# Kernel tuning notes

Hardware: AMD Instinct MI355X
Metric: run time of the kernel (lower is better)

The kernel has to match this reference:

```python
import jax, jax.numpy as jnp
import numpy as np

EPS = 1e-10

def setup_inputs() -> dict:
    key = jax.random.key(0)
    k1, k2, k3 = jax.random.split(key, 3)
    B, K, M, X, Y = 64, 4, 3, 256, 256
    predictions = jax.random.uniform(k1, (B, K, X, Y), dtype=jnp.float32)
    inputs = jax.random.normal(k2, (B, M, X, Y), dtype=jnp.float32)
    heart = jax.random.randint(k3, (B, 1, X, Y), 0, 2, dtype=jnp.int32)
    return {"predictions": predictions, "inputs": inputs, "heart": heart}

def reference(predictions, inputs, heart):
    B, K, X, Y = predictions.shape
    M = inputs.shape[1]
    P = X * Y
    pred = predictions.reshape(B, K, P)            # [B,K,P]
    inp = inputs.reshape(B, M, P)                  # [B,M,P]
    w = (heart.reshape(B, P) == 1).astype(pred.dtype)  # ROI mask [B,P]
    pw = pred * w[:, None, :]                      # masked responsibilities [B,K,P]
    s = pw.sum(-1) + EPS                           # [B,K]
    # weighted means/vars over masked pixels
    mu = jnp.einsum('bkp,bmp->bkm', pw, inp) / s[..., None]        # [B,K,M]
    diff = inp[:, None, :, :] - mu[..., None]                      # [B,K,M,P]
    var = jnp.einsum('bkmp,bkp->bkm', diff * diff, pw) / s[..., None] + EPS
    # per-channel Gaussian pdf, product over channels M
    pdf = jnp.exp(-diff * diff / (2.0 * var[..., None])) / jnp.sqrt(2.0 * jnp.pi * var)[..., None]
    temp = jnp.prod(pdf, axis=2)                   # [B,K,P]
    mix = jnp.sum(pred * temp, axis=1)             # [B,P]
    ll = jnp.log(mix + EPS)
    n = w.sum(-1)                                   # pixels in ROI per sample
    loss_b = -(ll * w).sum(-1) / n                 # mean over masked pixels
    return jnp.mean(loss_b)
```

## Files before the change

kernel.cpp:

```cpp
#include <hip/hip_runtime.h>

#define EPS 1e-10f

constexpr int B_ = 64, K_ = 4, M_ = 3, P_ = 65536;
constexpr int THREADS = 256;
constexpr int CHUNK = 2048;
constexpr int BPB = P_ / CHUNK;
constexpr int VPT = CHUNK / 4 / THREADS;
constexpr int NS = 32;
constexpr int NACC = 29;

__global__ __launch_bounds__(THREADS) void k_stats(
    const float* __restrict__ pred, const float* __restrict__ inp,
    const int* __restrict__ heart, float* __restrict__ sums)
{
    const int blk   = blockIdx.x;
    const int b     = blk / BPB;
    const int chunk = blk % BPB;
    const int tid   = threadIdx.x;

    const float4* pb = (const float4*)(pred + (size_t)b * K_ * P_);
    const float4* ib = (const float4*)(inp  + (size_t)b * M_ * P_);
    const int4*   hb = (const int4*)(heart + (size_t)b * P_);
    const int vbase = chunk * (CHUNK / 4);

    float sacc[K_], tacc[K_][M_], uacc[K_][M_], nacc = 0.f;
    #pragma unroll
    for (int k = 0; k < K_; ++k) {
        sacc[k] = 0.f;
        #pragma unroll
        for (int m = 0; m < M_; ++m) { tacc[k][m] = 0.f; uacc[k][m] = 0.f; }
    }

    #pragma unroll
    for (int it = 0; it < VPT; ++it) {
        const int v = vbase + it * THREADS + tid;
        const int4 h4 = hb[v];
        float4 pk[K_];
        float4 xm[M_];
        #pragma unroll
        for (int k = 0; k < K_; ++k) pk[k] = pb[k * (P_ / 4) + v];
        #pragma unroll
        for (int m = 0; m < M_; ++m) xm[m] = ib[m * (P_ / 4) + v];

        #define PIX1(C) do {                                                  \
            const float w = (h4.C == 1) ? 1.f : 0.f;                          \
            nacc += w;                                                        \
            _Pragma("unroll")                                                 \
            for (int k = 0; k < K_; ++k) {                                    \
                const float pw = pk[k].C * w;                                 \
                sacc[k] += pw;                                                \
                _Pragma("unroll")                                             \
                for (int m = 0; m < M_; ++m) {                                \
                    const float x = xm[m].C;                                  \
                    tacc[k][m] = fmaf(pw,     x, tacc[k][m]);                 \
                    uacc[k][m] = fmaf(pw * x, x, uacc[k][m]);                 \
                }                                                             \
            }                                                                 \
        } while (0)
        PIX1(x); PIX1(y); PIX1(z); PIX1(w);
        #undef PIX1
    }

    float acc[NACC];
    #pragma unroll
    for (int k = 0; k < K_; ++k) {
        acc[k] = sacc[k];
        #pragma unroll
        for (int m = 0; m < M_; ++m) {
            acc[4  + k * M_ + m] = tacc[k][m];
            acc[16 + k * M_ + m] = uacc[k][m];
        }
    }
    acc[28] = nacc;

    __shared__ float lds[4][NACC];
    const int lane = tid & 63, wid = tid >> 6;
    #pragma unroll
    for (int i = 0; i < NACC; ++i) {
        float x = acc[i];
        #pragma unroll
        for (int off = 32; off; off >>= 1) x += __shfl_down(x, off);
        if (lane == 0) lds[wid][i] = x;
    }
    __syncthreads();
    if (tid < NACC) {
        const float x = lds[0][tid] + lds[1][tid] + lds[2][tid] + lds[3][tid];
        atomicAdd(&sums[b * NS + tid], x);
    }
}

__global__ __launch_bounds__(THREADS) void k_loss(
    const float* __restrict__ pred, const float* __restrict__ inp,
    const int* __restrict__ heart, const float* __restrict__ sums,
    float* __restrict__ out)
{
    const int blk   = blockIdx.x;
    const int b     = blk / BPB;
    const int chunk = blk % BPB;
    const int tid   = threadIdx.x;

    const float* sb = sums + b * NS;
    float mu[K_][M_], iv[K_][M_], ck[K_];
    #pragma unroll
    for (int k = 0; k < K_; ++k) {
        const float s = sb[k] + EPS;
        const float inv_s = 1.f / s;
        float c = 1.f;
        #pragma unroll
        for (int m = 0; m < M_; ++m) {
            const float t = sb[4  + k * M_ + m];
            const float u = sb[16 + k * M_ + m];
            const float muv = t * inv_s;
            const float var = fmaf(-muv, muv, u * inv_s) + EPS;
            mu[k][m] = muv;
            iv[k][m] = 0.5f / var;
            c *= rsqrtf(6.283185307179586f * var);
        }
        ck[k] = c;
    }
    const float invn = 1.f / (sb[28] * (float)B_);

    const float4* pb = (const float4*)(pred + (size_t)b * K_ * P_);
    const float4* ib = (const float4*)(inp  + (size_t)b * M_ * P_);
    const int4*   hb = (const int4*)(heart + (size_t)b * P_);
    const int vbase = chunk * (CHUNK / 4);

    float part = 0.f;
    #pragma unroll
    for (int it = 0; it < VPT; ++it) {
        const int v = vbase + it * THREADS + tid;
        const int4 h4 = hb[v];
        float4 pk[K_];
        float4 xm[M_];
        #pragma unroll
        for (int k = 0; k < K_; ++k) pk[k] = pb[k * (P_ / 4) + v];
        #pragma unroll
        for (int m = 0; m < M_; ++m) xm[m] = ib[m * (P_ / 4) + v];

        #define PIX3(C) do {                                                  \
            const float w = (h4.C == 1) ? 1.f : 0.f;                          \
            float mix = EPS;                                                  \
            _Pragma("unroll")                                                 \
            for (int k = 0; k < K_; ++k) {                                    \
                float e = 0.f;                                                \
                _Pragma("unroll")                                             \
                for (int m = 0; m < M_; ++m) {                                \
                    const float d = xm[m].C - mu[k][m];                       \
                    e = fmaf(-(d * d), iv[k][m], e);                          \
                }                                                             \
                mix = fmaf(pk[k].C * ck[k], __expf(e), mix);                  \
            }                                                                 \
            part = fmaf(w, __logf(mix), part);                                \
        } while (0)
        PIX3(x); PIX3(y); PIX3(z); PIX3(w);
        #undef PIX3
    }

    __shared__ float lds[4];
    const int lane = tid & 63, wid = tid >> 6;
    float x = part;
    #pragma unroll
    for (int off = 32; off; off >>= 1) x += __shfl_down(x, off);
    if (lane == 0) lds[wid] = x;
    __syncthreads();
    if (tid == 0)
        atomicAdd(out, -(lds[0] + lds[1] + lds[2] + lds[3]) * invn);
}

extern "C" void kernel_launch(void* const* d_in, const int* in_sizes, int n_in,
                              void* d_out, int out_size, void* d_ws, size_t ws_size,
                              hipStream_t stream)
{
    const float* pred  = (const float*)d_in[0];
    const float* inp   = (const float*)d_in[1];
    const int*   heart = (const int*)d_in[2];
    float* out  = (float*)d_out;
    float* sums = (float*)d_ws;

    hipMemsetAsync(sums, 0, B_ * NS * sizeof(float), stream);
    hipMemsetAsync(out,  0, sizeof(float), stream);

    k_stats<<<B_ * BPB, THREADS, 0, stream>>>(pred, inp, heart, sums);
    k_loss <<<B_ * BPB, THREADS, 0, stream>>>(pred, inp, heart, sums, out);
}
```

Before: 76.10 us.

## Stage inputs through LDS with block-rotated plane order and smaller chunks

Both kernels now copy each 1024-pixel chunk of all eight planes (4 pred, 3 inp, heart) into shared memory. Each block starts at a different plane, chosen by a rotation from its block index, so concurrent blocks hit different DRAM channels and pages. Scheduling barriers keep the loads in issue order. The chunk is halved, so there are twice as many blocks and twice as many atomics. The extra LDS round-trip and 32KB of shared memory per block may reduce occupancy.

New measurement: 124.3 us. +63.4%, slower.

```diff
diff --git a/kernel.cpp b/kernel.cpp
--- a/kernel.cpp
+++ b/kernel.cpp
@@ -4,25 +4,48 @@
 
 constexpr int B_ = 64, K_ = 4, M_ = 3, P_ = 65536;
 constexpr int THREADS = 256;
-constexpr int CHUNK = 2048;
-constexpr int BPB = P_ / CHUNK;
-constexpr int VPT = CHUNK / 4 / THREADS;
+constexpr int CH = 1024;
+constexpr int NCH = P_ / CH;
 constexpr int NS = 32;
 constexpr int NACC = 29;
+
+__device__ __forceinline__ void stage_phases(
+    const float* __restrict__ pred, const float* __restrict__ inp,
+    const int* __restrict__ heart, int b, int px0, int rot,
+    float (*sbuf)[CH], int tid)
+{
+    #pragma unroll
+    for (int ph = 0; ph < 8; ++ph) {
+        const int pl = (ph + rot) & 7;
+        const float* g;
+        if (pl < 4)      g = pred + ((size_t)b * K_ + pl) * P_ + px0;
+        else if (pl < 7) g = inp  + ((size_t)b * M_ + (pl - 4)) * P_ + px0;
+        else             g = (const float*)(heart + (size_t)b * P_ + px0);
+        const float4 v = ((const float4*)g)[tid];
+        ((float4*)&sbuf[pl][0])[tid] = v;
+        __builtin_amdgcn_sched_barrier(0);
+    }
+}
 
 __global__ __launch_bounds__(THREADS) void k_stats(
     const float* __restrict__ pred, const float* __restrict__ inp,
     const int* __restrict__ heart, float* __restrict__ sums)
 {
-    const int blk   = blockIdx.x;
-    const int b     = blk / BPB;
-    const int chunk = blk % BPB;
+    __shared__ float sbuf[8][CH];
+    __shared__ float red[4][NACC];
+    const int b     = blockIdx.x / NCH;
+    const int chunk = blockIdx.x % NCH;
     const int tid   = threadIdx.x;
 
-    const float4* pb = (const float4*)(pred + (size_t)b * K_ * P_);
-    const float4* ib = (const float4*)(inp  + (size_t)b * M_ * P_);
-    const int4*   hb = (const int4*)(heart + (size_t)b * P_);
-    const int vbase = chunk * (CHUNK / 4);
+    stage_phases(pred, inp, heart, b, chunk * CH, blockIdx.x, sbuf, tid);
+    __syncthreads();
+
+    const int4 h4 = ((const int4*)&sbuf[7][0])[tid];
+    float4 pk[K_]; float4 xm[M_];
+    #pragma unroll
+    for (int k = 0; k < K_; ++k) pk[k] = ((const float4*)&sbuf[k][0])[tid];
+    #pragma unroll
+    for (int m = 0; m < M_; ++m) xm[m] = ((const float4*)&sbuf[4 + m][0])[tid];
 
     float sacc[K_], tacc[K_][M_], uacc[K_][M_], nacc = 0.f;
     #pragma unroll
@@ -32,35 +55,23 @@
         for (int m = 0; m < M_; ++m) { tacc[k][m] = 0.f; uacc[k][m] = 0.f; }
     }
 
-    #pragma unroll
-    for (int it = 0; it < VPT; ++it) {
-        const int v = vbase + it * THREADS + tid;
-        const int4 h4 = hb[v];
-        float4 pk[K_];
-        float4 xm[M_];
-        #pragma unroll
-        for (int k = 0; k < K_; ++k) pk[k] = pb[k * (P_ / 4) + v];
-        #pragma unroll
-        for (int m = 0; m < M_; ++m) xm[m] = ib[m * (P_ / 4) + v];
-
-        #define PIX1(C) do {                                                  \
-            const float w = (h4.C == 1) ? 1.f : 0.f;                          \
-            nacc += w;                                                        \
+    #define PIX1(C) do {                                                      \
+        const float w = (h4.C == 1) ? 1.f : 0.f;                              \
+        nacc += w;                                                            \
+        _Pragma("unroll")                                                     \
+        for (int k = 0; k < K_; ++k) {                                        \
+            const float pw = pk[k].C * w;                                     \
+            sacc[k] += pw;                                                    \
             _Pragma("unroll")                                                 \
-            for (int k = 0; k < K_; ++k) {                                    \
-                const float pw = pk[k].C * w;                                 \
-                sacc[k] += pw;                                                \
-                _Pragma("unroll")                                             \
-                for (int m = 0; m < M_; ++m) {                                \
-                    const float x = xm[m].C;                                  \
-                    tacc[k][m] = fmaf(pw,     x, tacc[k][m]);                 \
-                    uacc[k][m] = fmaf(pw * x, x, uacc[k][m]);                 \
-                }                                                             \
+            for (int m = 0; m < M_; ++m) {                                    \
+                const float x = xm[m].C;                                      \
+                tacc[k][m] = fmaf(pw,     x, tacc[k][m]);                     \
+                uacc[k][m] = fmaf(pw * x, x, uacc[k][m]);                     \
             }                                                                 \
-        } while (0)
-        PIX1(x); PIX1(y); PIX1(z); PIX1(w);
-        #undef PIX1
-    }
+        }                                                                     \
+    } while (0)
+    PIX1(x); PIX1(y); PIX1(z); PIX1(w);
+    #undef PIX1
 
     float acc[NACC];
     #pragma unroll
@@ -74,18 +85,17 @@
     }
     acc[28] = nacc;
 
-    __shared__ float lds[4][NACC];
     const int lane = tid & 63, wid = tid >> 6;
     #pragma unroll
     for (int i = 0; i < NACC; ++i) {
         float x = acc[i];
         #pragma unroll
         for (int off = 32; off; off >>= 1) x += __shfl_down(x, off);
-        if (lane == 0) lds[wid][i] = x;
+        if (lane == 0) red[wid][i] = x;
     }
     __syncthreads();
     if (tid < NACC) {
-        const float x = lds[0][tid] + lds[1][tid] + lds[2][tid] + lds[3][tid];
+        const float x = red[0][tid] + red[1][tid] + red[2][tid] + red[3][tid];
         atomicAdd(&sums[b * NS + tid], x);
     }
 }
@@ -95,9 +105,10 @@
     const int* __restrict__ heart, const float* __restrict__ sums,
     float* __restrict__ out)
 {
-    const int blk   = blockIdx.x;
-    const int b     = blk / BPB;
-    const int chunk = blk % BPB;
+    __shared__ float sbuf[8][CH];
+    __shared__ float red[4];
+    const int b     = blockIdx.x / NCH;
+    const int chunk = blockIdx.x % NCH;
     const int tid   = threadIdx.x;
 
     const float* sb = sums + b * NS;
@@ -121,51 +132,43 @@
     }
     const float invn = 1.f / (sb[28] * (float)B_);
 
-    const float4* pb = (const float4*)(pred + (size_t)b * K_ * P_);
-    const float4* ib = (const float4*)(inp  + (size_t)b * M_ * P_);
-    const int4*   hb = (const int4*)(heart + (size_t)b * P_);
-    const int vbase = chunk * (CHUNK / 4);
+    stage_phases(pred, inp, heart, b, chunk * CH, blockIdx.x, sbuf, tid);
+    __syncthreads();
+
+    const int4 h4 = ((const int4*)&sbuf[7][0])[tid];
+    float4 pk[K_]; float4 xm[M_];
+    #pragma unroll
+    for (int k = 0; k < K_; ++k) pk[k] = ((const float4*)&sbuf[k][0])[tid];
+    #pragma unroll
+    for (int m = 0; m < M_; ++m) xm[m] = ((const float4*)&sbuf[4 + m][0])[tid];
 
     float part = 0.f;
-    #pragma unroll
-    for (int it = 0; it < VPT; ++it) {
-        const int v = vbase + it * THREADS + tid;
-        const int4 h4 = hb[v];
-        float4 pk[K_];
-        float4 xm[M_];
-        #pragma unroll
-        for (int k = 0; k < K_; ++k) pk[k] = pb[k * (P_ / 4) + v];
-        #pragma unroll
-        for (int m = 0; m < M_; ++m) xm[m] = ib[m * (P_ / 4) + v];
+    #define PIX3(C) do {                                                      \
+        const float w = (h4.C == 1) ? 1.f : 0.f;                              \
+        float mix = EPS;                                                      \
+        _Pragma("unroll")                                                     \
+        for (int k = 0; k < K_; ++k) {                                        \
+            float e = 0.f;                                                    \
+            _Pragma("unroll")                                                 \
+            for (int m = 0; m < M_; ++m) {                                    \
+                const float d = xm[m].C - mu[k][m];                           \
+                e = fmaf(-(d * d), iv[k][m], e);                              \
+            }                                                                 \
+            mix = fmaf(pk[k].C * ck[k], __expf(e), mix);                      \
+        }                                                                     \
+        part = fmaf(w, __logf(mix), part);                                    \
+    } while (0)
+    PIX3(x); PIX3(y); PIX3(z); PIX3(w);
+    #undef PIX3
 
-        #define PIX3(C) do {                                                  \
-            const float w = (h4.C == 1) ? 1.f : 0.f;                          \
-            float mix = EPS;                                                  \
-            _Pragma("unroll")                                                 \
-            for (int k = 0; k < K_; ++k) {                                    \
-                float e = 0.f;                                                \
-                _Pragma("unroll")                                             \
-                for (int m = 0; m < M_; ++m) {                                \
-                    const float d = xm[m].C - mu[k][m];                       \
-                    e = fmaf(-(d * d), iv[k][m], e);                          \
-                }                                                             \
-                mix = fmaf(pk[k].C * ck[k], __expf(e), mix);                  \
-            }                                                                 \
-            part = fmaf(w, __logf(mix), part);                                \
-        } while (0)
-        PIX3(x); PIX3(y); PIX3(z); PIX3(w);
-        #undef PIX3
-    }
-
-    __shared__ float lds[4];
     const int lane = tid & 63, wid = tid >> 6;
     float x = part;
     #pragma unroll
     for (int off = 32; off; off >>= 1) x += __shfl_down(x, off);
-    if (lane == 0) lds[wid] = x;
+    if (lane == 0) red[wid] = x;
     __syncthreads();
     if (tid == 0)
-        atomicAdd(out, -(lds[0] + lds[1] + lds[2] + lds[3]) * invn);
+        atomicAdd(out, -(red[0] + red[1] + red[2] + red[3]) * invn);
 }
 
 extern "C" void kernel_launch(void* const* d_in, const int* in_sizes, int n_in,
@@ -181,6 +184,6 @@
     hipMemsetAsync(sums, 0, B_ * NS * sizeof(float), stream);
     hipMemsetAsync(out,  0, sizeof(float), stream);
 
-    k_stats<<<B_ * BPB, THREADS, 0, stream>>>(pred, inp, heart, sums);
-    k_loss <<<B_ * BPB, THREADS, 0, stream>>>(pred, inp, heart, sums, out);
+    k_stats<<<B_ * NCH, THREADS, 0, stream>>>(pred, inp, heart, sums);
+    k_loss <<<B_ * NCH, THREADS, 0, stream>>>(pred, inp, heart, sums, out);
 }
```
